# Kernel tuning notes

Hardware: AMD Instinct MI355X
Metric: run time of the kernel (lower is better)

## Reference

```python
import jax, jax.numpy as jnp
import numpy as np

N = 4096        # nodes
F_IN = 256      # in_features
F_OUT = 64      # out_features
H = 64          # lstm_out_features
MAX_DEG = 64    # max neighbor count == max packed seq length
ALPHA = 0.2     # leaky relu negative slope
NEG = -9e15


def setup_inputs() -> dict:
    key = jax.random.key(0)
    ks = jax.random.split(key, 8)
    h = jax.random.normal(ks[0], (N, F_IN), dtype=jnp.float32)
    # per-node neighbor counts in [1, MAX_DEG]
    seq_length = jax.random.randint(ks[1], (N,), 1, MAX_DEG + 1, dtype=jnp.int32)
    # adjacency with exactly seq_length[i] ones in row i
    r = jax.random.uniform(ks[2], (N, N))
    ranks = jnp.argsort(jnp.argsort(-r, axis=1), axis=1)
    adj = (ranks < seq_length[:, None]).astype(jnp.float32)
    # parameters (xavier-ish scale)
    W = jax.random.normal(ks[3], (F_IN, F_OUT), dtype=jnp.float32) * (2.0 / (F_IN + F_OUT)) ** 0.5
    a = jax.random.normal(ks[4], (2 * F_OUT, 1), dtype=jnp.float32) * 0.1
    # backward-direction LSTM weights (torch gate order i,f,g,o); forward dir is unused in output
    w_ih = jax.random.normal(ks[5], (4 * H, F_OUT), dtype=jnp.float32) * 0.1
    w_hh = jax.random.normal(ks[6], (4 * H, H), dtype=jnp.float32) * 0.1
    b_ih = jnp.zeros((4 * H,), dtype=jnp.float32)
    b_hh = jnp.zeros((4 * H,), dtype=jnp.float32)
    return {"h": h, "adj": adj, "seq_length": seq_length, "W": W, "a": a,
            "w_ih": w_ih, "w_hh": w_hh, "b_ih": b_ih, "b_hh": b_hh}


def reference(h, adj, seq_length, W, a, w_ih, w_hh, b_ih, b_hh):
    n = h.shape[0]
    Wh = h @ W                                   # [N, F_OUT]
    # e[i,j] = leakyrelu(a_left . Wh_i + a_right . Wh_j)  (same math as O(N^2) concat)
    a1, a2 = a[:F_OUT, 0], a[F_OUT:, 0]
    e = jax.nn.leaky_relu((Wh @ a1)[:, None] + (Wh @ a2)[None, :], negative_slope=ALPHA)
    att = jax.nn.softmax(jnp.where(adj > 0, e, NEG), axis=1)   # [N, N]
    Wh2 = att @ Wh                               # aggregated node features [N, F_OUT]
    # sort neighbors by descending attention; LSTM only reads the first seq_length[i] <= MAX_DEG
    order = jnp.argsort(-att, axis=1)[:, :MAX_DEG]            # [N, T]
    seq = Wh2[order]                              # [N, T, F_OUT]
    # backward LSTM direction == run forward over the length-reversed sequence
    t = jnp.arange(MAX_DEG)
    rev_idx = jnp.clip(seq_length[:, None] - 1 - t[None, :], 0)
    rev = jnp.take_along_axis(seq, rev_idx[:, :, None], axis=1)  # [N, T, F_OUT]
    mask = t[None, :] < seq_length[:, None]                       # [N, T]

    def cell(carry, xm):
        hs, cs = carry
        x, m = xm                                 # x: [N, F_OUT], m: [N]
        gates = x @ w_ih.T + hs @ w_hh.T + b_ih + b_hh
        i, f, g, o = jnp.split(gates, 4, axis=1)
        c_new = jax.nn.sigmoid(f) * cs + jax.nn.sigmoid(i) * jnp.tanh(g)
        h_new = jax.nn.sigmoid(o) * jnp.tanh(c_new)
        m = m[:, None]
        return (jnp.where(m, h_new, hs), jnp.where(m, c_new, cs)), None

    init = (jnp.zeros((n, H), Wh.dtype), jnp.zeros((n, H), Wh.dtype))
    xs = (jnp.swapaxes(rev, 0, 1), mask.T)        # time-major
    (hn, _), _ = jax.lax.scan(cell, init, xs)
    return hn                                     # [N, H]  == torch hn[-1] (backward dir)
```

## Files before the change

kernel.cpp:

```cpp
#include <hip/hip_runtime.h>
#include <hip/hip_bf16.h>
#include <math.h>

#define N_NODES 4096
#define F_INN   256
#define F_OUTT  64
#define HID     64
#define MAXDEG  64

typedef __attribute__((ext_vector_type(8))) short bf16x8;
typedef __attribute__((ext_vector_type(4))) float f32x4;

__device__ int    g_mode;
__device__ int    g_anyArr[64];
__device__ float  g_Wh [N_NODES * F_OUTT];
__device__ float  g_s1 [N_NODES];
__device__ float  g_s2 [N_NODES];
__device__ int    g_rev[N_NODES * MAXDEG];
__device__ int    g_perm[N_NODES];
__device__ float4 g_GX [N_NODES * F_OUTT];

__device__ __forceinline__ float bf2f(unsigned short u) {
  union { unsigned int i; float f; } v; v.i = ((unsigned int)u) << 16; return v.f;
}
__device__ __forceinline__ unsigned short f2bf(float f) {
  union { __hip_bfloat16 b; unsigned short u; } v; v.b = __float2bfloat16(f); return v.u;
}

__device__ __forceinline__ float bcastf(float v, int l) {
  return __int_as_float(__builtin_amdgcn_readlane(__float_as_int(v), l));
}

__device__ __forceinline__ float rcp_fast(float x) { return __builtin_amdgcn_rcpf(x); }

__device__ __forceinline__ float sigm(float x) {
  return rcp_fast(1.f + __expf(-x));
}
__device__ __forceinline__ float tanh_fast(float x) {
  return fmaf(-2.f, rcp_fast(1.f + __expf(2.f * x)), 1.f);
}

__device__ __forceinline__ int mbcnt64(unsigned long long m) {
  return __builtin_amdgcn_mbcnt_hi((unsigned)(m >> 32),
         __builtin_amdgcn_mbcnt_lo((unsigned)(m & 0xFFFFFFFFull), 0));
}

__device__ __forceinline__ bf16x8 zfrag() {
  bf16x8 z;
  #pragma unroll
  for (int i = 0; i < 8; i++) z[i] = 0;
  return z;
}

__device__ __forceinline__ void block_sync_lds() {
  __asm__ volatile("s_waitcnt lgkmcnt(0)" ::: "memory");
  __builtin_amdgcn_s_barrier();
}

#define MFMA16(a, b, c) __builtin_amdgcn_mfma_f32_16x16x32_bf16((a), (b), (c), 0, 0, 0)

__global__ __launch_bounds__(256) void k_detect(const unsigned int* __restrict__ aw) {
  __shared__ int any;
  if (threadIdx.x == 0) any = 0;
  __syncthreads();
  const uint4 v = ((const uint4*)aw)[blockIdx.x * 256 + threadIdx.x];
  int loc = (int)((v.x & 0xFFFFu) | (v.y & 0xFFFFu) | (v.z & 0xFFFFu) | (v.w & 0xFFFFu));
  if (loc) atomicOr(&any, 1);
  __syncthreads();
  if (threadIdx.x == 0) g_anyArr[blockIdx.x] = any;
}

__global__ __launch_bounds__(256) void k_sort(const int* __restrict__ seq) {
  __shared__ int hist[MAXDEG + 1];
  __shared__ int offs[MAXDEG + 1];
  const int tid = threadIdx.x;
  if (tid <= MAXDEG) hist[tid] = 0;
  __syncthreads();
  if (tid == 0) {
    int any = 0;
    for (int b = 0; b < 64; b++) any |= g_anyArr[b];
    g_mode = any ? 1 : 0;
  }
  for (int i = tid; i < N_NODES; i += 256)
    atomicAdd(&hist[min(max(seq[i], 0), MAXDEG)], 1);
  __syncthreads();
  if (tid == 0) {
    int run = 0;
    for (int L = MAXDEG; L >= 0; L--) { offs[L] = run; run += hist[L]; }
  }
  __syncthreads();
  for (int i = tid; i < N_NODES; i += 256) {
    int p = atomicAdd(&offs[min(max(seq[i], 0), MAXDEG)], 1);
    g_perm[p] = i;
  }
}

__global__ __launch_bounds__(256) void k_wh(
    const void* __restrict__ h, const void* __restrict__ W, const void* __restrict__ a)
{
  const bool bf16 = (g_mode == 1);
  __shared__ float Ws[F_INN * F_OUTT];
  const int tid = threadIdx.x;
  if (bf16) {
    const ushort4* Wu = (const ushort4*)W;
    for (int v = tid; v < F_INN * F_OUTT / 4; v += 256) {
      ushort4 u = Wu[v];
      ((float4*)Ws)[v] = make_float4(bf2f(u.x), bf2f(u.y), bf2f(u.z), bf2f(u.w));
    }
  } else {
    const float4* Wf = (const float4*)W;
    for (int v = tid; v < F_INN * F_OUTT / 4; v += 256) ((float4*)Ws)[v] = Wf[v];
  }
  __syncthreads();
  const int wave = tid >> 6, lane = tid & 63;
  const int row = blockIdx.x * 4 + wave;
  float hr0, hr1, hr2, hr3;
  if (bf16) {
    ushort4 v = ((const ushort4*)((const unsigned short*)h + row * F_INN))[lane];
    hr0 = bf2f(v.x); hr1 = bf2f(v.y); hr2 = bf2f(v.z); hr3 = bf2f(v.w);
  } else {
    float4 v = ((const float4*)((const float*)h + row * F_INN))[lane];
    hr0 = v.x; hr1 = v.y; hr2 = v.z; hr3 = v.w;
  }
  double acc = 0.0;
  #pragma unroll 8
  for (int l = 0; l < 64; l++) {
    float h0 = bcastf(hr0, l), h1 = bcastf(hr1, l);
    float h2 = bcastf(hr2, l), h3 = bcastf(hr3, l);
    acc += (double)h0 * (double)Ws[(l * 4 + 0) * F_OUTT + lane];
    acc += (double)h1 * (double)Ws[(l * 4 + 1) * F_OUTT + lane];
    acc += (double)h2 * (double)Ws[(l * 4 + 2) * F_OUTT + lane];
    acc += (double)h3 * (double)Ws[(l * 4 + 3) * F_OUTT + lane];
  }
  const float whv = (float)acc;
  g_Wh[row * F_OUTT + lane] = whv;
  float a1, a2;
  if (bf16) {
    a1 = bf2f(((const unsigned short*)a)[lane]);
    a2 = bf2f(((const unsigned short*)a)[F_OUTT + lane]);
  } else {
    a1 = ((const float*)a)[lane];
    a2 = ((const float*)a)[F_OUTT + lane];
  }
  double t1 = (double)whv * (double)a1;
  double t2 = (double)whv * (double)a2;
  #pragma unroll
  for (int off = 32; off > 0; off >>= 1) {
    t1 += __shfl_down(t1, off);
    t2 += __shfl_down(t2, off);
  }
  if (lane == 0) { g_s1[row] = (float)t1; g_s2[row] = (float)t2; }
}

__global__ __launch_bounds__(256) void k_att(
    const void* __restrict__ adj, const void* __restrict__ w_ih,
    const void* __restrict__ b_ih, const void* __restrict__ b_hh)
{
  const bool bf16 = (g_mode == 1);
  const int wv = threadIdx.x >> 6, lane = threadIdx.x & 63;
  const int i = blockIdx.x * 4 + wv;

  __shared__ int   s_nbr[4][MAXDEG];
  __shared__ float s_att[4][MAXDEG];
  __shared__ int   s_srt[4][MAXDEG];
  __shared__ float s_wh2[4][F_OUTT];
  int*   nbr  = s_nbr[wv];
  float* attp = s_att[wv];
  int*   srt  = s_srt[wv];
  float* wh2  = s_wh2[wv];

  int base = 0;
  if (bf16) {
    const uint4* ar = (const uint4*)((const unsigned short*)adj + (size_t)i * N_NODES);
    #pragma unroll
    for (int it = 0; it < 8; it++) {
      const uint4 v = ar[it * 64 + lane];
      unsigned word[4] = {v.x, v.y, v.z, v.w};
      bool nz[8];
      #pragma unroll
      for (int k = 0; k < 4; k++) {
        nz[2 * k]     = (word[k] & 0x0000FFFFu) != 0u;
        nz[2 * k + 1] = (word[k] & 0xFFFF0000u) != 0u;
      }
      int pre = 0, tot = 0;
      #pragma unroll
      for (int k = 0; k < 8; k++) {
        unsigned long long bl = __ballot(nz[k]);
        pre += mbcnt64(bl);
        tot += __popcll(bl);
      }
      int loc = 0;
      #pragma unroll
      for (int k = 0; k < 8; k++) {
        if (nz[k]) {
          int p = base + pre + loc;
          if (p < MAXDEG) nbr[p] = it * 512 + lane * 8 + k;
          loc++;
        }
      }
      base += tot;
    }
  } else {
    const float4* ar = (const float4*)((const float*)adj + (size_t)i * N_NODES);
    #pragma unroll
    for (int it = 0; it < 16; it++) {
      const float4 v = ar[it * 64 + lane];
      bool nz[4] = {v.x != 0.0f, v.y != 0.0f, v.z != 0.0f, v.w != 0.0f};
      int pre = 0, tot = 0;
      #pragma unroll
      for (int k = 0; k < 4; k++) {
        unsigned long long bl = __ballot(nz[k]);
        pre += mbcnt64(bl);
        tot += __popcll(bl);
      }
      int loc = 0;
      #pragma unroll
      for (int k = 0; k < 4; k++) {
        if (nz[k]) {
          int p = base + pre + loc;
          if (p < MAXDEG) nbr[p] = it * 256 + lane * 4 + k;
          loc++;
        }
      }
      base += tot;
    }
  }
  const int L = min(base, MAXDEG);

  const int   jn  = (lane < L) ? nbr[lane] : 0;
  const float s2v = g_s2[jn];
  {
    float s = g_s1[i] + s2v;
    float e = (s > 0.0f) ? s : 0.2f * s;
    if (lane >= L) e = -3.0e38f;
    float m = e;
    #pragma unroll
    for (int off = 32; off > 0; off >>= 1) m = fmaxf(m, __shfl_xor(m, off));
    float p = (lane < L) ? __expf(e - m) : 0.0f;
    float ssum = p;
    #pragma unroll
    for (int off = 32; off > 0; off >>= 1) ssum += __shfl_xor(ssum, off);
    const float av = p * rcp_fast(ssum);
    attp[lane] = av;
    int rank = 0;
    for (int qq = 0; qq < L; qq++) {
      float aq = __shfl(av, qq);
      int   jq = __shfl(jn, qq);
      rank += (aq > av || (aq == av && jq < jn)) ? 1 : 0;
    }
    if (lane < L) srt[rank] = jn;
  }
  g_rev[i * MAXDEG + lane] = (lane < L) ? srt[L - 1 - lane] : 0;

  float a0 = 0.f, a1 = 0.f, a2 = 0.f, a3 = 0.f;
  int q = 0;
  for (; q + 4 <= L; q += 4) {
    const int j0 = nbr[q], j1 = nbr[q + 1], j2 = nbr[q + 2], j3 = nbr[q + 3];
    const float t0 = attp[q], t1 = attp[q + 1], t2 = attp[q + 2], t3 = attp[q + 3];
    a0 = fmaf(t0, g_Wh[(size_t)j0 * F_OUTT + lane], a0);
    a1 = fmaf(t1, g_Wh[(size_t)j1 * F_OUTT + lane], a1);
    a2 = fmaf(t2, g_Wh[(size_t)j2 * F_OUTT + lane], a2);
    a3 = fmaf(t3, g_Wh[(size_t)j3 * F_OUTT + lane], a3);
  }
  for (; q < L; q++) {
    const int j0 = nbr[q];
    a0 = fmaf(attp[q], g_Wh[(size_t)j0 * F_OUTT + lane], a0);
  }
  wh2[lane] = (a0 + a1) + (a2 + a3);

  float gx[4] = {0.f, 0.f, 0.f, 0.f};
  if (bf16) {
    #pragma unroll
    for (int g = 0; g < 4; g++) {
      const unsigned short* wr = (const unsigned short*)w_ih + (size_t)(g * 64 + lane) * F_OUTT;
      #pragma unroll
      for (int ch = 0; ch < 8; ch++) {
        bf16x8 vv = *(const bf16x8*)(wr + ch * 8);
        #pragma unroll
        for (int e2 = 0; e2 < 8; e2++)
          gx[g] = fmaf(bf2f((unsigned short)vv[e2]), wh2[ch * 8 + e2], gx[g]);
      }
      gx[g] += bf2f(((const unsigned short*)b_ih)[g * 64 + lane]) +
               bf2f(((const unsigned short*)b_hh)[g * 64 + lane]);
    }
  } else {
    #pragma unroll
    for (int g = 0; g < 4; g++) {
      const float* wr = (const float*)w_ih + (size_t)(g * 64 + lane) * F_OUTT;
      #pragma unroll
      for (int ch = 0; ch < 16; ch++) {
        float4 vv = *(const float4*)(wr + ch * 4);
        gx[g] = fmaf(vv.x, wh2[ch * 4 + 0], gx[g]);
        gx[g] = fmaf(vv.y, wh2[ch * 4 + 1], gx[g]);
        gx[g] = fmaf(vv.z, wh2[ch * 4 + 2], gx[g]);
        gx[g] = fmaf(vv.w, wh2[ch * 4 + 3], gx[g]);
      }
      gx[g] += ((const float*)b_ih)[g * 64 + lane] + ((const float*)b_hh)[g * 64 + lane];
    }
  }
  g_GX[(size_t)i * F_OUTT + lane] = make_float4(gx[0], gx[1], gx[2], gx[3]);
}

__global__ __launch_bounds__(256, 1) void k_lstm_mfma(
    const void* __restrict__ w_hh, const int* __restrict__ seq,
    void* __restrict__ out)
{
  const bool bf16 = (g_mode == 1);
  __shared__ __align__(16) unsigned short lds_h[2][16 * 72];
  __shared__ int lds_idx[16][MAXDEG];
  const int tid = threadIdx.x;
  const int w = tid >> 6, lane = tid & 63;
  const int q = lane >> 4, c = lane & 15;
  const int rb = blockIdx.x * 16;

  for (int v = tid; v < 16 * MAXDEG; v += 256) {
    const int e = v >> 6, t0 = v & (MAXDEG - 1);
    const int row = g_perm[rb + e] & (N_NODES - 1);
    lds_idx[e][t0] = g_rev[row * MAXDEG + t0] & (N_NODES - 1);
  }

  const int Lmax = min(max(seq[g_perm[rb] & (N_NODES - 1)], 0), MAXDEG);
  int row_e[4], Ls_e[4];
  #pragma unroll
  for (int r = 0; r < 4; r++) {
    row_e[r] = g_perm[rb + q * 4 + r] & (N_NODES - 1);
    Ls_e[r]  = min(max(seq[row_e[r]], 0), MAXDEG);
  }
  const int d_unit = 16 * w + c;

  bf16x8 Bhi[4][2];
  #pragma unroll
  for (int g = 0; g < 4; g++) {
    const int col = 64 * g + d_unit;
    #pragma unroll
    for (int ch = 0; ch < 2; ch++) {
      if (bf16) {
        Bhi[g][ch] = *(const bf16x8*)((const unsigned short*)w_hh + (size_t)col * 64 + ch * 32 + q * 8);
      } else {
        const float* wp = (const float*)w_hh + (size_t)col * 64 + ch * 32 + q * 8;
        float4 va = *(const float4*)wp, vb = *(const float4*)(wp + 4);
        bf16x8 f;
        f[0] = (short)f2bf(va.x); f[1] = (short)f2bf(va.y);
        f[2] = (short)f2bf(va.z); f[3] = (short)f2bf(va.w);
        f[4] = (short)f2bf(vb.x); f[5] = (short)f2bf(vb.y);
        f[6] = (short)f2bf(vb.z); f[7] = (short)f2bf(vb.w);
        Bhi[g][ch] = f;
      }
    }
  }

  __syncthreads();

  float4 gxb[4][4];
  #pragma unroll
  for (int s = 0; s < 4; s++) {
    #pragma unroll
    for (int r = 0; r < 4; r++)
      gxb[s][r] = g_GX[lds_idx[q * 4 + r][s] * F_OUTT + d_unit];
  }
  int idx_cur[4];
  #pragma unroll
  for (int r = 0; r < 4; r++) idx_cur[r] = lds_idx[q * 4 + r][4];

  bf16x8 h0 = zfrag(), h1 = zfrag();
  float cst[4] = {0.f, 0.f, 0.f, 0.f}, hst[4] = {0.f, 0.f, 0.f, 0.f};
  const int Lr = (Lmax + 3) & ~3;

  for (int t = 0; t < Lr; t += 4) {
    #pragma unroll
    for (int j = 0; j < 4; j++) {
      const int tt = t + j;
      f32x4 acc[4];
      #pragma unroll
      for (int g = 0; g < 4; g++) {
        f32x4 a;
        a[0] = (g==0)?gxb[j][0].x:(g==1)?gxb[j][0].y:(g==2)?gxb[j][0].z:gxb[j][0].w;
        a[1] = (g==0)?gxb[j][1].x:(g==1)?gxb[j][1].y:(g==2)?gxb[j][1].z:gxb[j][1].w;
        a[2] = (g==0)?gxb[j][2].x:(g==1)?gxb[j][2].y:(g==2)?gxb[j][2].z:gxb[j][2].w;
        a[3] = (g==0)?gxb[j][3].x:(g==1)?gxb[j][3].y:(g==2)?gxb[j][3].z:gxb[j][3].w;
        a = MFMA16(h0, Bhi[g][0], a);
        a = MFMA16(h1, Bhi[g][1], a);
        acc[g] = a;
      }
      #pragma unroll
      for (int r = 0; r < 4; r++)
        gxb[j][r] = g_GX[idx_cur[r] * F_OUTT + d_unit];
      {
        const int nt = min(tt + 5, MAXDEG - 1);
        #pragma unroll
        for (int r = 0; r < 4; r++) idx_cur[r] = lds_idx[q * 4 + r][nt];
      }
      unsigned short* lh = lds_h[j & 1];
      #pragma unroll
      for (int r = 0; r < 4; r++) {
        float ig = sigm(acc[0][r]);
        float fg = sigm(acc[1][r]);
        float gg = tanh_fast(acc[2][r]);
        float og = sigm(acc[3][r]);
        float cn = fg * cst[r] + ig * gg;
        float hn = og * tanh_fast(cn);
        bool live = (tt < Ls_e[r]);
        cst[r] = live ? cn : cst[r];
        hst[r] = live ? hn : hst[r];
        lh[(q * 4 + r) * 72 + d_unit] = f2bf(hst[r]);
      }
      block_sync_lds();
      {
        const unsigned short* lr_ = lds_h[j & 1] + c * 72;
        h0 = *(const bf16x8*)(lr_ + 8 * q);
        h1 = *(const bf16x8*)(lr_ + 32 + 8 * q);
      }
    }
  }
  #pragma unroll
  for (int r = 0; r < 4; r++) {
    if (bf16) ((__hip_bfloat16*)out)[row_e[r] * HID + d_unit] = __float2bfloat16(hst[r]);
    else      ((float*)out)[row_e[r] * HID + d_unit] = hst[r];
  }
}

extern "C" void kernel_launch(void* const* d_in, const int* in_sizes, int n_in,
                              void* d_out, int out_size, void* d_ws, size_t ws_size,
                              hipStream_t stream) {
  (void)in_sizes; (void)n_in; (void)out_size; (void)d_ws; (void)ws_size;
  const void* h    = d_in[0];
  const void* adj  = d_in[1];
  const int*  seq  = (const int*)d_in[2];
  const void* W    = d_in[3];
  const void* a    = d_in[4];
  const void* w_ih = d_in[5];
  const void* w_hh = d_in[6];
  const void* b_ih = d_in[7];
  const void* b_hh = d_in[8];

  k_detect   <<<64,           256, 0, stream>>>((const unsigned int*)adj);
  k_sort     <<<1,            256, 0, stream>>>(seq);
  k_wh       <<<N_NODES / 4,  256, 0, stream>>>(h, W, a);
  k_att      <<<N_NODES / 4,  256, 0, stream>>>(adj, w_ih, b_ih, b_hh);
  k_lstm_mfma<<<N_NODES / 16, 256, 0, stream>>>(w_hh, seq, d_out);
}
```

Measured before the change: 233.5 us.

## Split adjacency scan into separate per-row kernel with four waves per row

Moves the adjacency-row nonzero compaction out of the attention kernel into a new kernel where each row is scanned by a full block of four waves, each covering a quarter of the row, with the segments merged through shared memory. The attention kernel then reads compacted neighbor lists and counts from global buffers. The aim is more memory-level parallelism on the 64 MB adjacency read, which was previously serialized in one wave per row. The cost is an extra launch plus a global write and read of the neighbor lists.

```diff
diff --git a/kernel.cpp b/kernel.cpp
--- a/kernel.cpp
+++ b/kernel.cpp
@@ -18,6 +18,8 @@
 __device__ float  g_s2 [N_NODES];
 __device__ int    g_rev[N_NODES * MAXDEG];
 __device__ int    g_perm[N_NODES];
+__device__ int    g_nbr[N_NODES * MAXDEG];
+__device__ int    g_cnt[N_NODES];
 __device__ float4 g_GX [N_NODES * F_OUTT];
 
 __device__ __forceinline__ float bf2f(unsigned short u) {
@@ -93,6 +95,83 @@
     int p = atomicAdd(&offs[min(max(seq[i], 0), MAXDEG)], 1);
     g_perm[p] = i;
   }
+}
+
+__global__ __launch_bounds__(256) void k_scan(const void* __restrict__ adj) {
+  const bool bf16 = (g_mode == 1);
+  const int i = blockIdx.x;
+  const int w = threadIdx.x >> 6, lane = threadIdx.x & 63;
+  __shared__ int seg[4][MAXDEG];
+  __shared__ int scnt[4];
+
+  int base = 0;
+  if (bf16) {
+    const uint4* ar = (const uint4*)((const unsigned short*)adj + (size_t)i * N_NODES);
+    #pragma unroll
+    for (int it = 0; it < 2; it++) {
+      const uint4 v = ar[w * 128 + it * 64 + lane];
+      unsigned word[4] = {v.x, v.y, v.z, v.w};
+      bool nz[8];
+      #pragma unroll
+      for (int k = 0; k < 4; k++) {
+        nz[2 * k]     = (word[k] & 0x0000FFFFu) != 0u;
+        nz[2 * k + 1] = (word[k] & 0xFFFF0000u) != 0u;
+      }
+      int pre = 0, tot = 0;
+      #pragma unroll
+      for (int k = 0; k < 8; k++) {
+        unsigned long long bl = __ballot(nz[k]);
+        pre += mbcnt64(bl);
+        tot += __popcll(bl);
+      }
+      int loc = 0;
+      #pragma unroll
+      for (int k = 0; k < 8; k++) {
+        if (nz[k]) {
+          int p = base + pre + loc;
+          if (p < MAXDEG) seg[w][p] = w * 1024 + it * 512 + lane * 8 + k;
+          loc++;
+        }
+      }
+      base += tot;
+    }
+  } else {
+    const float4* ar = (const float4*)((const float*)adj + (size_t)i * N_NODES);
+    #pragma unroll
+    for (int it = 0; it < 4; it++) {
+      const float4 v = ar[w * 256 + it * 64 + lane];
+      bool nz[4] = {v.x != 0.0f, v.y != 0.0f, v.z != 0.0f, v.w != 0.0f};
+      int pre = 0, tot = 0;
+      #pragma unroll
+      for (int k = 0; k < 4; k++) {
+        unsigned long long bl = __ballot(nz[k]);
+        pre += mbcnt64(bl);
+        tot += __popcll(bl);
+      }
+      int loc = 0;
+      #pragma unroll
+      for (int k = 0; k < 4; k++) {
+        if (nz[k]) {
+          int p = base + pre + loc;
+          if (p < MAXDEG) seg[w][p] = w * 1024 + it * 256 + lane * 4 + k;
+          loc++;
+        }
+      }
+      base += tot;
+    }
+  }
+  if (lane == 0) scnt[w] = base;
+  __syncthreads();
+  int off = 0;
+  #pragma unroll
+  for (int u = 0; u < 4; u++) off += (u < w) ? scnt[u] : 0;
+  const int cw = min(scnt[w], MAXDEG);
+  if (lane < cw) {
+    const int p = off + lane;
+    if (p < MAXDEG) g_nbr[i * MAXDEG + p] = seg[w][lane];
+  }
+  if (threadIdx.x == 0)
+    g_cnt[i] = min(scnt[0] + scnt[1] + scnt[2] + scnt[3], MAXDEG);
 }
 
 __global__ __launch_bounds__(256) void k_wh(
@@ -152,8 +231,8 @@
   if (lane == 0) { g_s1[row] = (float)t1; g_s2[row] = (float)t2; }
 }
 
-__global__ __launch_bounds__(256) void k_att(
-    const void* __restrict__ adj, const void* __restrict__ w_ih,
+__global__ __launch_bounds__(256) void k_att2(
+    const void* __restrict__ w_ih,
     const void* __restrict__ b_ih, const void* __restrict__ b_hh)
 {
   const bool bf16 = (g_mode == 1);
@@ -169,66 +248,13 @@
   int*   srt  = s_srt[wv];
   float* wh2  = s_wh2[wv];
 
-  int base = 0;
-  if (bf16) {
-    const uint4* ar = (const uint4*)((const unsigned short*)adj + (size_t)i * N_NODES);
-    #pragma unroll
-    for (int it = 0; it < 8; it++) {
-      const uint4 v = ar[it * 64 + lane];
-      unsigned word[4] = {v.x, v.y, v.z, v.w};
-      bool nz[8];
-      #pragma unroll
-      for (int k = 0; k < 4; k++) {
-        nz[2 * k]     = (word[k] & 0x0000FFFFu) != 0u;
-        nz[2 * k + 1] = (word[k] & 0xFFFF0000u) != 0u;
-      }
-      int pre = 0, tot = 0;
-      #pragma unroll
-      for (int k = 0; k < 8; k++) {
-        unsigned long long bl = __ballot(nz[k]);
-        pre += mbcnt64(bl);
-        tot += __popcll(bl);
-      }
-      int loc = 0;
-      #pragma unroll
-      for (int k = 0; k < 8; k++) {
-        if (nz[k]) {
-          int p = base + pre + loc;
-          if (p < MAXDEG) nbr[p] = it * 512 + lane * 8 + k;
-          loc++;
-        }
-      }
-      base += tot;
-    }
-  } else {
-    const float4* ar = (const float4*)((const float*)adj + (size_t)i * N_NODES);
-    #pragma unroll
-    for (int it = 0; it < 16; it++) {
-      const float4 v = ar[it * 64 + lane];
-      bool nz[4] = {v.x != 0.0f, v.y != 0.0f, v.z != 0.0f, v.w != 0.0f};
-      int pre = 0, tot = 0;
-      #pragma unroll
-      for (int k = 0; k < 4; k++) {
-        unsigned long long bl = __ballot(nz[k]);
-        pre += mbcnt64(bl);
-        tot += __popcll(bl);
-      }
-      int loc = 0;
-      #pragma unroll
-      for (int k = 0; k < 4; k++) {
-        if (nz[k]) {
-          int p = base + pre + loc;
-          if (p < MAXDEG) nbr[p] = it * 256 + lane * 4 + k;
-          loc++;
-        }
-      }
-      base += tot;
-    }
-  }
-  const int L = min(base, MAXDEG);
-
-  const int   jn  = (lane < L) ? nbr[lane] : 0;
+  const int L = min(g_cnt[i], MAXDEG);
+  int jn = 0;
+  if (lane < L) jn = g_nbr[i * MAXDEG + lane] & (N_NODES - 1);
+  nbr[lane] = jn;
+
   const float s2v = g_s2[jn];
+  float av;
   {
     float s = g_s1[i] + s2v;
     float e = (s > 0.0f) ? s : 0.2f * s;
@@ -240,7 +266,7 @@
     float ssum = p;
     #pragma unroll
     for (int off = 32; off > 0; off >>= 1) ssum += __shfl_xor(ssum, off);
-    const float av = p * rcp_fast(ssum);
+    av = p * rcp_fast(ssum);
     attp[lane] = av;
     int rank = 0;
     for (int qq = 0; qq < L; qq++) {
@@ -435,7 +461,8 @@
 
   k_detect   <<<64,           256, 0, stream>>>((const unsigned int*)adj);
   k_sort     <<<1,            256, 0, stream>>>(seq);
+  k_scan     <<<N_NODES,      256, 0, stream>>>(adj);
   k_wh       <<<N_NODES / 4,  256, 0, stream>>>(h, W, a);
-  k_att      <<<N_NODES / 4,  256, 0, stream>>>(adj, w_ih, b_ih, b_hh);
+  k_att2     <<<N_NODES / 4,  256, 0, stream>>>(w_ih, b_ih, b_hh);
   k_lstm_mfma<<<N_NODES / 16, 256, 0, stream>>>(w_hh, seq, d_out);
 }
```

After: 227.4 us. -2.6%, faster.
